# Kernel tuning notes

Hardware: AMD Instinct MI355X
Metric: run time of the kernel (lower is better)

Reference implementation:

```python
import jax, jax.numpy as jnp
import numpy as np

N = 6144
IN_DIM = 256
HID = 64
HEADS = 4
LAT = 32
ALPHA = 0.2  # LeakyReLU negative slope
NEG_INF = -9e15


def setup_inputs() -> dict:
    key = jax.random.key(0)
    ks = jax.random.split(key, 6)
    x = jax.random.normal(ks[0], (N, IN_DIM), jnp.float32)
    # sparse symmetric 0/1 adjacency, avg degree ~ 25
    A = (jax.random.uniform(ks[1], (N, N)) < 0.004).astype(jnp.float32)
    A = jnp.maximum(A, A.T)
    # xavier-uniform-ish params, matching pyGAT GraphAttentionLayer shapes
    s1 = float(np.sqrt(6.0 / (IN_DIM + HID)))
    W_heads = jax.random.uniform(ks[2], (HEADS, IN_DIM, HID), jnp.float32, -s1, s1)
    sa = float(np.sqrt(6.0 / (2 * HID + 1)))
    a_heads = jax.random.uniform(ks[3], (HEADS, 2 * HID), jnp.float32, -sa, sa)
    s2 = float(np.sqrt(6.0 / (HEADS * HID + LAT)))
    W_out = jax.random.uniform(ks[4], (HEADS * HID, LAT), jnp.float32, -s2, s2)
    sb = float(np.sqrt(6.0 / (2 * LAT + 1)))
    a_out = jax.random.uniform(ks[5], (2 * LAT,), jnp.float32, -sb, sb)
    return {"x": x, "A": A, "W_heads": W_heads, "a_heads": a_heads,
            "W_out": W_out, "a_out": a_out}


def _gat_layer(h, adj_mask, W, a, concat):
    # h: [N, F_in], W: [F_in, F], a: [2F]
    Wh = h @ W                              # [N, F]
    f = W.shape[1]
    e_src = Wh @ a[:f]                      # [N]
    e_dst = Wh @ a[f:]                      # [N]
    e = jax.nn.leaky_relu(e_src[:, None] + e_dst[None, :], ALPHA)  # [N, N]
    e = jnp.where(adj_mask, e, NEG_INF)
    att = jax.nn.softmax(e, axis=1)         # masked softmax over neighbors
    out = att @ Wh                          # [N, F]
    return jax.nn.elu(out) if concat else out


def reference(x, A, W_heads, a_heads, W_out, a_out):
    # normalize(A, 'sym', False): D^{-1/2} A D^{-1/2}
    deg = A.sum(axis=1)
    dinv = jnp.where(deg > 0, deg ** -0.5, 0.0)
    An = A * dinv[:, None] * dinv[None, :]
    mask = An > 0
    heads = [_gat_layer(x, mask, W_heads[i], a_heads[i], True) for i in range(HEADS)]
    h = jnp.concatenate(heads, axis=1)      # [N, HEADS*HID]
    z = jax.nn.elu(_gat_layer(h, mask, W_out, a_out, False))  # [N, LAT]
    return jax.nn.sigmoid(z @ z.T)          # [N, N]
```

## Files before the change

kernel.cpp:

```cpp
#include <hip/hip_runtime.h>
#include <hip/hip_bf16.h>

#define NN 6144
#define IN_DIM 256
#define HID 64
#define HEADS 4
#define LAT 32
#define CAP 192
#define ALPHA 0.2f
#define GEMM_BLOCKS 384
#define WSTRIDE 264

typedef __attribute__((ext_vector_type(8))) short bf16x8;
typedef __attribute__((ext_vector_type(4))) float f32x4;

__device__ __forceinline__ float elu_f(float v)   { return v > 0.f ? v : expm1f(v); }
__device__ __forceinline__ float lrelu_f(float v) { return v > 0.f ? v : ALPHA * v; }

__device__ __forceinline__ void split_bf16(float v, unsigned short& hi, unsigned short& lo) {
    unsigned u = __builtin_bit_cast(unsigned, v);
    hi = (unsigned short)(u >> 16);
    float vh = __builtin_bit_cast(float, u & 0xFFFF0000u);
    float rl = v - vh;
    lo = (unsigned short)(__builtin_bit_cast(unsigned, rl) >> 16);
}
__device__ __forceinline__ unsigned short f2bf(float f) {
    unsigned u = __builtin_bit_cast(unsigned, f);
    return (unsigned short)((u + 0x7FFFu + ((u >> 16) & 1u)) >> 16);
}
__device__ __forceinline__ float bf2f(unsigned short b) {
    return __builtin_bit_cast(float, (unsigned)b << 16);
}

__global__ __launch_bounds__(256) void k_pre(const float* __restrict__ A,
                                             const float* __restrict__ x,
                                             const float* __restrict__ Wheads,
                                             const float* __restrict__ aheads,
                                             int* __restrict__ nbr, int* __restrict__ cnt,
                                             unsigned short* __restrict__ Whb,
                                             float* __restrict__ es4, float* __restrict__ ed4) {
    __shared__ __align__(16) float smem[2048];
    int bid = blockIdx.x;
    int t = threadIdx.x;
    if (bid < GEMM_BLOCKS) {
        int head = bid & 3, m0 = (bid >> 2) * 64;
        float (*As)[64] = (float(*)[64])smem;
        float (*Bs)[64] = (float(*)[64])(smem + 1024);
        const float* Wc = Wheads + (size_t)head * IN_DIM * HID;
        int ty = t >> 4, tx = t & 15;
        float acc[4][4] = {};
        for (int k0 = 0; k0 < IN_DIM; k0 += 16) {
            {
                int row = t >> 2, k4 = (t & 3) * 4;
                float4 v = *(const float4*)(x + (size_t)(m0 + row) * IN_DIM + k0 + k4);
                As[k4 + 0][row] = v.x; As[k4 + 1][row] = v.y;
                As[k4 + 2][row] = v.z; As[k4 + 3][row] = v.w;
                int kk = t >> 4, n4 = (t & 15) * 4;
                *(float4*)&Bs[kk][n4] = *(const float4*)(Wc + (size_t)(k0 + kk) * HID + n4);
            }
            __syncthreads();
            #pragma unroll
            for (int k = 0; k < 16; ++k) {
                float4 av = *(float4*)&As[k][ty * 4];
                float4 bv = *(float4*)&Bs[k][tx * 4];
                float ar[4] = {av.x, av.y, av.z, av.w};
                float br[4] = {bv.x, bv.y, bv.z, bv.w};
                #pragma unroll
                for (int i = 0; i < 4; ++i)
                    #pragma unroll
                    for (int j = 0; j < 4; ++j)
                        acc[i][j] = fmaf(ar[i], br[j], acc[i][j]);
            }
            __syncthreads();
        }
        #pragma unroll
        for (int i = 0; i < 4; ++i) {
            ushort4 o;
            o.x = f2bf(acc[i][0]); o.y = f2bf(acc[i][1]);
            o.z = f2bf(acc[i][2]); o.w = f2bf(acc[i][3]);
            *(ushort4*)(Whb + (size_t)(m0 + ty * 4 + i) * (HEADS * HID) + head * HID + tx * 4) = o;
        }
        float4 a1v = *(const float4*)(aheads + head * 2 * HID + tx * 4);
        float4 a2v = *(const float4*)(aheads + head * 2 * HID + HID + tx * 4);
        #pragma unroll
        for (int i = 0; i < 4; ++i) {
            float p1 = acc[i][0] * a1v.x + acc[i][1] * a1v.y + acc[i][2] * a1v.z + acc[i][3] * a1v.w;
            float p2 = acc[i][0] * a2v.x + acc[i][1] * a2v.y + acc[i][2] * a2v.z + acc[i][3] * a2v.w;
            #pragma unroll
            for (int off = 8; off; off >>= 1) {
                p1 += __shfl_down(p1, off, 16);
                p2 += __shfl_down(p2, off, 16);
            }
            if (tx == 0) {
                es4[(size_t)(m0 + ty * 4 + i) * 4 + head] = p1;
                ed4[(size_t)(m0 + ty * 4 + i) * 4 + head] = p2;
            }
        }
    } else {
        int row = bid - GEMM_BLOCKS;
        int* lcnt = (int*)smem;
        const float4* Arow = (const float4*)(A + (size_t)row * NN);
        if (t == 0) *lcnt = 0;
        __syncthreads();
        int* my = nbr + (size_t)row * CAP;
        #pragma unroll
        for (int it = 0; it < NN / 4 / 256; ++it) {
            int idx4 = it * 256 + t;
            float4 v = Arow[idx4];
            int base = idx4 * 4;
            if (v.x != 0.f) { int p = atomicAdd(lcnt, 1); if (p < CAP) my[p] = base; }
            if (v.y != 0.f) { int p = atomicAdd(lcnt, 1); if (p < CAP) my[p] = base + 1; }
            if (v.z != 0.f) { int p = atomicAdd(lcnt, 1); if (p < CAP) my[p] = base + 2; }
            if (v.w != 0.f) { int p = atomicAdd(lcnt, 1); if (p < CAP) my[p] = base + 3; }
        }
        __syncthreads();
        if (t == 0) cnt[row] = *lcnt < CAP ? *lcnt : CAP;
    }
}

__global__ __launch_bounds__(256, 4) void k_attn1g2(const int* __restrict__ nbr, const int* __restrict__ cnt,
                                                    const float4* __restrict__ es4, const float4* __restrict__ ed4,
                                                    const unsigned short* __restrict__ Whb,
                                                    const float* __restrict__ Wout, const float* __restrict__ aout,
                                                    float* __restrict__ Wh2,
                                                    float* __restrict__ es2, float* __restrict__ ed2) {
    __shared__ int colS[4][CAP];
    __shared__ __align__(16) float attH[4][HEADS][CAP];
    __shared__ __align__(16) unsigned short hbf[4][WSTRIDE];
    __shared__ __align__(16) unsigned short WoutT[LAT][WSTRIDE];
    int w = threadIdx.x >> 6, l = threadIdx.x & 63;
    int i = blockIdx.x * 4 + w;
    int c = cnt[i];
    const int* nb = nbr + (size_t)i * CAP;

    #pragma unroll
    for (int it = 0; it < 8; ++it) {
        int q = it * 256 + threadIdx.x;
        float4 v = *(const float4*)(Wout + q * 4);
        int trow = q >> 3, c0 = (q * 4) & 31;
        WoutT[c0 + 0][trow] = f2bf(v.x);
        WoutT[c0 + 1][trow] = f2bf(v.y);
        WoutT[c0 + 2][trow] = f2bf(v.z);
        WoutT[c0 + 3][trow] = f2bf(v.w);
    }

    float4 esv = es4[i];
    float s0 = 0.f, s1 = 0.f, s2 = 0.f, s3 = 0.f;
    for (int j = l; j < c; j += 64) {
        int cj = nb[j];
        colS[w][j] = cj;
        float4 edv = ed4[cj];
        float4 e;
        e.x = __expf(lrelu_f(esv.x + edv.x));
        e.y = __expf(lrelu_f(esv.y + edv.y));
        e.z = __expf(lrelu_f(esv.z + edv.z));
        e.w = __expf(lrelu_f(esv.w + edv.w));
        attH[w][0][j] = e.x; attH[w][1][j] = e.y;
        attH[w][2][j] = e.z; attH[w][3][j] = e.w;
        s0 += e.x; s1 += e.y; s2 += e.z; s3 += e.w;
    }
    #pragma unroll
    for (int off = 32; off; off >>= 1) {
        s0 += __shfl_down(s0, off); s1 += __shfl_down(s1, off);
        s2 += __shfl_down(s2, off); s3 += __shfl_down(s3, off);
    }
    s0 = __shfl(s0, 0); s1 = __shfl(s1, 0); s2 = __shfl(s2, 0); s3 = __shfl(s3, 0);

    int hd = l >> 4;
    float sh = hd < 2 ? (hd == 0 ? s0 : s1) : (hd == 2 ? s2 : s3);
    float invh = 1.0f / sh;
    float4 hv;
    if (c == 0) {
        float a0 = 0.f, a1 = 0.f, a2 = 0.f, a3 = 0.f;
        for (int r = 0; r < NN; ++r) {
            ushort4 v = *(const ushort4*)(Whb + (size_t)r * (HEADS * HID) + 4 * l);
            a0 += bf2f(v.x); a1 += bf2f(v.y); a2 += bf2f(v.z); a3 += bf2f(v.w);
        }
        hv.x = elu_f(a0 / NN); hv.y = elu_f(a1 / NN);
        hv.z = elu_f(a2 / NN); hv.w = elu_f(a3 / NN);
    } else {
        const unsigned short* Wb = Whb + 4 * l;
        float ax[8], ay[8], az[8], aw[8];
        #pragma unroll
        for (int k = 0; k < 8; ++k) { ax[k] = 0.f; ay[k] = 0.f; az[k] = 0.f; aw[k] = 0.f; }
        int j = 0;
        for (; j + 8 <= c; j += 8) {
            float4 f0 = *(float4*)&attH[w][hd][j];
            float4 f1 = *(float4*)&attH[w][hd][j + 4];
            int4 c0v = *(int4*)&colS[w][j];
            int4 c1v = *(int4*)&colS[w][j + 4];
            float ff[8] = {f0.x, f0.y, f0.z, f0.w, f1.x, f1.y, f1.z, f1.w};
            int   cj[8] = {c0v.x, c0v.y, c0v.z, c0v.w, c1v.x, c1v.y, c1v.z, c1v.w};
            ushort4 vv[8];
            #pragma unroll
            for (int k = 0; k < 8; ++k) vv[k] = *(const ushort4*)(Wb + (size_t)cj[k] * (HEADS * HID));
            #pragma unroll
            for (int k = 0; k < 8; ++k) {
                ax[k] = fmaf(ff[k], bf2f(vv[k].x), ax[k]);
                ay[k] = fmaf(ff[k], bf2f(vv[k].y), ay[k]);
                az[k] = fmaf(ff[k], bf2f(vv[k].z), az[k]);
                aw[k] = fmaf(ff[k], bf2f(vv[k].w), aw[k]);
            }
        }
        for (; j < c; ++j) {
            int cj = colS[w][j];
            float f = attH[w][hd][j];
            ushort4 v = *(const ushort4*)(Wb + (size_t)cj * (HEADS * HID));
            ax[0] = fmaf(f, bf2f(v.x), ax[0]); ay[0] = fmaf(f, bf2f(v.y), ay[0]);
            az[0] = fmaf(f, bf2f(v.z), az[0]); aw[0] = fmaf(f, bf2f(v.w), aw[0]);
        }
        float rx = ((ax[0] + ax[1]) + (ax[2] + ax[3])) + ((ax[4] + ax[5]) + (ax[6] + ax[7]));
        float ry = ((ay[0] + ay[1]) + (ay[2] + ay[3])) + ((ay[4] + ay[5]) + (ay[6] + ay[7]));
        float rz = ((az[0] + az[1]) + (az[2] + az[3])) + ((az[4] + az[5]) + (az[6] + az[7]));
        float rw = ((aw[0] + aw[1]) + (aw[2] + aw[3])) + ((aw[4] + aw[5]) + (aw[6] + aw[7]));
        hv.x = elu_f(rx * invh); hv.y = elu_f(ry * invh);
        hv.z = elu_f(rz * invh); hv.w = elu_f(rw * invh);
    }
    {
        ushort4 o;
        o.x = f2bf(hv.x); o.y = f2bf(hv.y); o.z = f2bf(hv.z); o.w = f2bf(hv.w);
        *(ushort4*)&hbf[w][4 * l] = o;
    }
    __syncthreads();

    {
        int r = l & 15, kg = l >> 4;
        f32x4 accA = {0.f, 0.f, 0.f, 0.f};
        f32x4 accB = {0.f, 0.f, 0.f, 0.f};
        #pragma unroll
        for (int k0 = 0; k0 < 8; ++k0) {
            bf16x8 af = {0, 0, 0, 0, 0, 0, 0, 0};
            if (r < 4) af = *(const bf16x8*)&hbf[r][k0 * 32 + kg * 8];
            bf16x8 b0 = *(const bf16x8*)&WoutT[r][k0 * 32 + kg * 8];
            bf16x8 b1 = *(const bf16x8*)&WoutT[16 + r][k0 * 32 + kg * 8];
            accA = __builtin_amdgcn_mfma_f32_16x16x32_bf16(af, b0, accA, 0, 0, 0);
            accB = __builtin_amdgcn_mfma_f32_16x16x32_bf16(af, b1, accB, 0, 0, 0);
        }
        float v0 = (w == 0) ? accA[0] : (w == 1) ? accA[1] : (w == 2) ? accA[2] : accA[3];
        float v1 = (w == 0) ? accB[0] : (w == 1) ? accB[1] : (w == 2) ? accB[2] : accB[3];
        if (l < 16) {
            Wh2[(size_t)i * LAT + l]      = v0;
            Wh2[(size_t)i * LAT + 16 + l] = v1;
            float p1 = v0 * aout[l] + v1 * aout[16 + l];
            float p2 = v0 * aout[32 + l] + v1 * aout[48 + l];
            #pragma unroll
            for (int off = 8; off; off >>= 1) {
                p1 += __shfl_down(p1, off, 16);
                p2 += __shfl_down(p2, off, 16);
            }
            if (l == 0) { es2[i] = p1; ed2[i] = p2; }
        }
    }
}

__global__ __launch_bounds__(256, 8) void k_attn2(const int* __restrict__ nbr, const int* __restrict__ cnt,
                                                  const float* __restrict__ es2, const float* __restrict__ ed2,
                                                  const float* __restrict__ Wh2,
                                                  unsigned short* __restrict__ zh, unsigned short* __restrict__ zl) {
    __shared__ float att[4][CAP];
    __shared__ int col[4][CAP];
    int w = threadIdx.x >> 6, l = threadIdx.x & 63;
    int i = blockIdx.x * 4 + w;
    int c = cnt[i];
    if (c == 0) {
        if (l < LAT) {
            float s = 0.f;
            for (int r = 0; r < NN; ++r) s += Wh2[(size_t)r * LAT + l];
            unsigned short hi, lo;
            split_bf16(elu_f(s * (1.0f / NN)), hi, lo);
            zh[(size_t)i * LAT + l] = hi;
            zl[(size_t)i * LAT + l] = lo;
        }
        return;
    }
    float esi = es2[i];
    const int* nb = nbr + (size_t)i * CAP;
    float s = 0.f;
    for (int j = l; j < c; j += 64) {
        int cj = nb[j];
        col[w][j] = cj;
        float p = __expf(lrelu_f(esi + ed2[cj]));
        att[w][j] = p;
        s += p;
    }
    #pragma unroll
    for (int off = 32; off; off >>= 1) s += __shfl_down(s, off);
    s = __shfl(s, 0);
    if (l < LAT) {
        float inv = 1.0f / s;
        float a0 = 0.f, a1 = 0.f, a2 = 0.f, a3 = 0.f;
        int j = 0;
        for (; j + 4 <= c; j += 4) {
            a0 = fmaf(att[w][j + 0], Wh2[(size_t)col[w][j + 0] * LAT + l], a0);
            a1 = fmaf(att[w][j + 1], Wh2[(size_t)col[w][j + 1] * LAT + l], a1);
            a2 = fmaf(att[w][j + 2], Wh2[(size_t)col[w][j + 2] * LAT + l], a2);
            a3 = fmaf(att[w][j + 3], Wh2[(size_t)col[w][j + 3] * LAT + l], a3);
        }
        for (; j < c; ++j)
            a0 = fmaf(att[w][j], Wh2[(size_t)col[w][j] * LAT + l], a0);
        unsigned short hi, lo;
        split_bf16(elu_f(((a0 + a1) + (a2 + a3)) * inv), hi, lo);
        zh[(size_t)i * LAT + l] = hi;
        zl[(size_t)i * LAT + l] = lo;
    }
}

__global__ __launch_bounds__(256, 8) void k_zzt(const unsigned short* __restrict__ zh,
                                                const unsigned short* __restrict__ zl,
                                                float* __restrict__ out) {
    int t = threadIdx.x, w = t >> 6, l = t & 63;
    int m0 = blockIdx.y * 64 + w * 16;
    int n0 = blockIdx.x * 64;
    int r = l & 15, kg = (l >> 4) * 8;
    bf16x8 ah = *(const bf16x8*)(zh + (size_t)(m0 + r) * LAT + kg);
    bf16x8 al = *(const bf16x8*)(zl + (size_t)(m0 + r) * LAT + kg);
    int mbase = m0 + (l >> 4) * 4;
    #pragma unroll
    for (int jp = 0; jp < 2; ++jp) {
        int nbA = n0 + (jp * 2 + 0) * 16;
        int nbB = n0 + (jp * 2 + 1) * 16;
        bf16x8 bhA = *(const bf16x8*)(zh + (size_t)(nbA + r) * LAT + kg);
        bf16x8 blA = *(const bf16x8*)(zl + (size_t)(nbA + r) * LAT + kg);
        bf16x8 bhB = *(const bf16x8*)(zh + (size_t)(nbB + r) * LAT + kg);
        bf16x8 blB = *(const bf16x8*)(zl + (size_t)(nbB + r) * LAT + kg);
        f32x4 accA = {0.f, 0.f, 0.f, 0.f};
        accA = __builtin_amdgcn_mfma_f32_16x16x32_bf16(ah, bhA, accA, 0, 0, 0);
        accA = __builtin_amdgcn_mfma_f32_16x16x32_bf16(ah, blA, accA, 0, 0, 0);
        accA = __builtin_amdgcn_mfma_f32_16x16x32_bf16(al, bhA, accA, 0, 0, 0);
        f32x4 accB = {0.f, 0.f, 0.f, 0.f};
        accB = __builtin_amdgcn_mfma_f32_16x16x32_bf16(ah, bhB, accB, 0, 0, 0);
        accB = __builtin_amdgcn_mfma_f32_16x16x32_bf16(ah, blB, accB, 0, 0, 0);
        accB = __builtin_amdgcn_mfma_f32_16x16x32_bf16(al, bhB, accB, 0, 0, 0);
        float4 oA, oB;
        oA.x = 1.0f / (1.0f + __expf(-accA[0]));
        oA.y = 1.0f / (1.0f + __expf(-accA[1]));
        oA.z = 1.0f / (1.0f + __expf(-accA[2]));
        oA.w = 1.0f / (1.0f + __expf(-accA[3]));
        oB.x = 1.0f / (1.0f + __expf(-accB[0]));
        oB.y = 1.0f / (1.0f + __expf(-accB[1]));
        oB.z = 1.0f / (1.0f + __expf(-accB[2]));
        oB.w = 1.0f / (1.0f + __expf(-accB[3]));
        *(float4*)(out + (size_t)(nbA + (l & 15)) * NN + mbase) = oA;
        *(float4*)(out + (size_t)(nbB + (l & 15)) * NN + mbase) = oB;
    }
}

extern "C" void kernel_launch(void* const* d_in, const int* in_sizes, int n_in,
                              void* d_out, int out_size, void* d_ws, size_t ws_size,
                              hipStream_t stream) {
    const float* x      = (const float*)d_in[0];
    const float* A      = (const float*)d_in[1];
    const float* Wheads = (const float*)d_in[2];
    const float* aheads = (const float*)d_in[3];
    const float* Wout   = (const float*)d_in[4];
    const float* aout   = (const float*)d_in[5];
    float* out = (float*)d_out;

    char* ws = (char*)d_ws;
    size_t o = 0;
    auto alloc = [&](size_t bytes) { void* p = ws + o; o += (bytes + 255) & ~(size_t)255; return p; };
    int*   nbr   = (int*)  alloc((size_t)NN * CAP * 4);
    int*   cnt   = (int*)  alloc((size_t)NN * 4);
    unsigned short* Whb = (unsigned short*)alloc((size_t)NN * HEADS * HID * 2);
    float* es4   = (float*)alloc((size_t)NN * 4 * 4);
    float* ed4   = (float*)alloc((size_t)NN * 4 * 4);
    float* Wh2   = (float*)alloc((size_t)NN * LAT * 4);
    float* es2   = (float*)alloc((size_t)NN * 4);
    float* ed2   = (float*)alloc((size_t)NN * 4);
    unsigned short* zh = (unsigned short*)alloc((size_t)NN * LAT * 2);
    unsigned short* zl = (unsigned short*)alloc((size_t)NN * LAT * 2);

    k_pre     <<<GEMM_BLOCKS + NN, 256, 0, stream>>>(A, x, Wheads, aheads, nbr, cnt, Whb, es4, ed4);
    k_attn1g2 <<<NN / 4, 256, 0, stream>>>(nbr, cnt, (const float4*)es4, (const float4*)ed4,
                                           Whb, Wout, aout, Wh2, es2, ed2);
    k_attn2   <<<NN / 4, 256, 0, stream>>>(nbr, cnt, es2, ed2, Wh2, zh, zl);
    k_zzt     <<<dim3(NN / 64, NN / 64), 256, 0, stream>>>(zh, zl, out);
}
```

Measured before the change: 108.1 us.

## Precompute bf16 Wout transpose in k_pre and shrink attention blocks to two waves

The bf16 transpose of Wout moves out of every k_attn1g2 block into one extra k_pre block that writes it to global memory once. k_attn1g2 then uses 128-thread blocks (two rows), keeps attention weights as bf16 in shared memory, drops the block barrier, reads Wout tiles straight from global/L2, and uses a 4-way instead of 8-way gather unroll. The aim is to cut redundant per-block transpose work and shared-memory footprint so occupancy rises. The trade-offs are extra rounding of attention weights to bf16, less memory-level parallelism per wave in the gather, and MFMA B operands fetched from global instead of LDS.

```diff
diff --git a/kernel.cpp b/kernel.cpp
--- a/kernel.cpp
+++ b/kernel.cpp
@@ -9,7 +9,6 @@
 #define CAP 192
 #define ALPHA 0.2f
 #define GEMM_BLOCKS 384
-#define WSTRIDE 264
 
 typedef __attribute__((ext_vector_type(8))) short bf16x8;
 typedef __attribute__((ext_vector_type(4))) float f32x4;
@@ -36,9 +35,11 @@
                                              const float* __restrict__ x,
                                              const float* __restrict__ Wheads,
                                              const float* __restrict__ aheads,
+                                             const float* __restrict__ Wout,
                                              int* __restrict__ nbr, int* __restrict__ cnt,
                                              unsigned short* __restrict__ Whb,
-                                             float* __restrict__ es4, float* __restrict__ ed4) {
+                                             float* __restrict__ es4, float* __restrict__ ed4,
+                                             unsigned short* __restrict__ WoutT) {
     __shared__ __align__(16) float smem[2048];
     int bid = blockIdx.x;
     int t = threadIdx.x;
@@ -96,7 +97,7 @@
                 ed4[(size_t)(m0 + ty * 4 + i) * 4 + head] = p2;
             }
         }
-    } else {
+    } else if (bid < GEMM_BLOCKS + NN) {
         int row = bid - GEMM_BLOCKS;
         int* lcnt = (int*)smem;
         const float4* Arow = (const float4*)(A + (size_t)row * NN);
@@ -115,34 +116,32 @@
         }
         __syncthreads();
         if (t == 0) cnt[row] = *lcnt < CAP ? *lcnt : CAP;
-    }
-}
-
-__global__ __launch_bounds__(256, 4) void k_attn1g2(const int* __restrict__ nbr, const int* __restrict__ cnt,
+    } else {
+        #pragma unroll
+        for (int cq = 0; cq < 8; ++cq) {
+            float4 v = *(const float4*)(Wout + t * LAT + cq * 4);
+            WoutT[(cq * 4 + 0) * IN_DIM + t] = f2bf(v.x);
+            WoutT[(cq * 4 + 1) * IN_DIM + t] = f2bf(v.y);
+            WoutT[(cq * 4 + 2) * IN_DIM + t] = f2bf(v.z);
+            WoutT[(cq * 4 + 3) * IN_DIM + t] = f2bf(v.w);
+        }
+    }
+}
+
+__global__ __launch_bounds__(128, 8) void k_attn1g2(const int* __restrict__ nbr, const int* __restrict__ cnt,
                                                     const float4* __restrict__ es4, const float4* __restrict__ ed4,
                                                     const unsigned short* __restrict__ Whb,
-                                                    const float* __restrict__ Wout, const float* __restrict__ aout,
+                                                    const unsigned short* __restrict__ WoutT,
+                                                    const float* __restrict__ aout,
                                                     float* __restrict__ Wh2,
                                                     float* __restrict__ es2, float* __restrict__ ed2) {
-    __shared__ int colS[4][CAP];
-    __shared__ __align__(16) float attH[4][HEADS][CAP];
-    __shared__ __align__(16) unsigned short hbf[4][WSTRIDE];
-    __shared__ __align__(16) unsigned short WoutT[LAT][WSTRIDE];
+    __shared__ int colS[2][CAP];
+    __shared__ __align__(16) unsigned short attB[2][HEADS][CAP];
+    __shared__ __align__(16) unsigned short hr[2][HEADS * HID];
     int w = threadIdx.x >> 6, l = threadIdx.x & 63;
-    int i = blockIdx.x * 4 + w;
+    int i = blockIdx.x * 2 + w;
     int c = cnt[i];
     const int* nb = nbr + (size_t)i * CAP;
-
-    #pragma unroll
-    for (int it = 0; it < 8; ++it) {
-        int q = it * 256 + threadIdx.x;
-        float4 v = *(const float4*)(Wout + q * 4);
-        int trow = q >> 3, c0 = (q * 4) & 31;
-        WoutT[c0 + 0][trow] = f2bf(v.x);
-        WoutT[c0 + 1][trow] = f2bf(v.y);
-        WoutT[c0 + 2][trow] = f2bf(v.z);
-        WoutT[c0 + 3][trow] = f2bf(v.w);
-    }
 
     float4 esv = es4[i];
     float s0 = 0.f, s1 = 0.f, s2 = 0.f, s3 = 0.f;
@@ -150,14 +149,13 @@
         int cj = nb[j];
         colS[w][j] = cj;
         float4 edv = ed4[cj];
-        float4 e;
-        e.x = __expf(lrelu_f(esv.x + edv.x));
-        e.y = __expf(lrelu_f(esv.y + edv.y));
-        e.z = __expf(lrelu_f(esv.z + edv.z));
-        e.w = __expf(lrelu_f(esv.w + edv.w));
-        attH[w][0][j] = e.x; attH[w][1][j] = e.y;
-        attH[w][2][j] = e.z; attH[w][3][j] = e.w;
-        s0 += e.x; s1 += e.y; s2 += e.z; s3 += e.w;
+        float ex = __expf(lrelu_f(esv.x + edv.x));
+        float ey = __expf(lrelu_f(esv.y + edv.y));
+        float ez = __expf(lrelu_f(esv.z + edv.z));
+        float ew = __expf(lrelu_f(esv.w + edv.w));
+        attB[w][0][j] = f2bf(ex); attB[w][1][j] = f2bf(ey);
+        attB[w][2][j] = f2bf(ez); attB[w][3][j] = f2bf(ew);
+        s0 += ex; s1 += ey; s2 += ez; s3 += ew;
     }
     #pragma unroll
     for (int off = 32; off; off >>= 1) {
@@ -180,22 +178,20 @@
         hv.z = elu_f(a2 / NN); hv.w = elu_f(a3 / NN);
     } else {
         const unsigned short* Wb = Whb + 4 * l;
-        float ax[8], ay[8], az[8], aw[8];
-        #pragma unroll
-        for (int k = 0; k < 8; ++k) { ax[k] = 0.f; ay[k] = 0.f; az[k] = 0.f; aw[k] = 0.f; }
+        float ax[4], ay[4], az[4], aw[4];
+        #pragma unroll
+        for (int k = 0; k < 4; ++k) { ax[k] = 0.f; ay[k] = 0.f; az[k] = 0.f; aw[k] = 0.f; }
         int j = 0;
-        for (; j + 8 <= c; j += 8) {
-            float4 f0 = *(float4*)&attH[w][hd][j];
-            float4 f1 = *(float4*)&attH[w][hd][j + 4];
-            int4 c0v = *(int4*)&colS[w][j];
-            int4 c1v = *(int4*)&colS[w][j + 4];
-            float ff[8] = {f0.x, f0.y, f0.z, f0.w, f1.x, f1.y, f1.z, f1.w};
-            int   cj[8] = {c0v.x, c0v.y, c0v.z, c0v.w, c1v.x, c1v.y, c1v.z, c1v.w};
-            ushort4 vv[8];
-            #pragma unroll
-            for (int k = 0; k < 8; ++k) vv[k] = *(const ushort4*)(Wb + (size_t)cj[k] * (HEADS * HID));
-            #pragma unroll
-            for (int k = 0; k < 8; ++k) {
+        for (; j + 4 <= c; j += 4) {
+            ushort4 fB = *(ushort4*)&attB[w][hd][j];
+            int4 cv = *(int4*)&colS[w][j];
+            float ff[4] = {bf2f(fB.x), bf2f(fB.y), bf2f(fB.z), bf2f(fB.w)};
+            int   cj[4] = {cv.x, cv.y, cv.z, cv.w};
+            ushort4 vv[4];
+            #pragma unroll
+            for (int k = 0; k < 4; ++k) vv[k] = *(const ushort4*)(Wb + (size_t)cj[k] * (HEADS * HID));
+            #pragma unroll
+            for (int k = 0; k < 4; ++k) {
                 ax[k] = fmaf(ff[k], bf2f(vv[k].x), ax[k]);
                 ay[k] = fmaf(ff[k], bf2f(vv[k].y), ay[k]);
                 az[k] = fmaf(ff[k], bf2f(vv[k].z), az[k]);
@@ -204,24 +200,21 @@
         }
         for (; j < c; ++j) {
             int cj = colS[w][j];
-            float f = attH[w][hd][j];
+            float f = bf2f(attB[w][hd][j]);
             ushort4 v = *(const ushort4*)(Wb + (size_t)cj * (HEADS * HID));
             ax[0] = fmaf(f, bf2f(v.x), ax[0]); ay[0] = fmaf(f, bf2f(v.y), ay[0]);
             az[0] = fmaf(f, bf2f(v.z), az[0]); aw[0] = fmaf(f, bf2f(v.w), aw[0]);
         }
-        float rx = ((ax[0] + ax[1]) + (ax[2] + ax[3])) + ((ax[4] + ax[5]) + (ax[6] + ax[7]));
-        float ry = ((ay[0] + ay[1]) + (ay[2] + ay[3])) + ((ay[4] + ay[5]) + (ay[6] + ay[7]));
-        float rz = ((az[0] + az[1]) + (az[2] + az[3])) + ((az[4] + az[5]) + (az[6] + az[7]));
-        float rw = ((aw[0] + aw[1]) + (aw[2] + aw[3])) + ((aw[4] + aw[5]) + (aw[6] + aw[7]));
-        hv.x = elu_f(rx * invh); hv.y = elu_f(ry * invh);
-        hv.z = elu_f(rz * invh); hv.w = elu_f(rw * invh);
+        hv.x = elu_f(((ax[0] + ax[1]) + (ax[2] + ax[3])) * invh);
+        hv.y = elu_f(((ay[0] + ay[1]) + (ay[2] + ay[3])) * invh);
+        hv.z = elu_f(((az[0] + az[1]) + (az[2] + az[3])) * invh);
+        hv.w = elu_f(((aw[0] + aw[1]) + (aw[2] + aw[3])) * invh);
     }
     {
         ushort4 o;
         o.x = f2bf(hv.x); o.y = f2bf(hv.y); o.z = f2bf(hv.z); o.w = f2bf(hv.w);
-        *(ushort4*)&hbf[w][4 * l] = o;
-    }
-    __syncthreads();
+        *(ushort4*)&hr[w][4 * l] = o;
+    }
 
     {
         int r = l & 15, kg = l >> 4;
@@ -230,15 +223,14 @@
         #pragma unroll
         for (int k0 = 0; k0 < 8; ++k0) {
             bf16x8 af = {0, 0, 0, 0, 0, 0, 0, 0};
-            if (r < 4) af = *(const bf16x8*)&hbf[r][k0 * 32 + kg * 8];
-            bf16x8 b0 = *(const bf16x8*)&WoutT[r][k0 * 32 + kg * 8];
-            bf16x8 b1 = *(const bf16x8*)&WoutT[16 + r][k0 * 32 + kg * 8];
+            if (r == 0) af = *(const bf16x8*)&hr[w][k0 * 32 + kg * 8];
+            bf16x8 b0 = *(const bf16x8*)(WoutT + (size_t)r * IN_DIM + k0 * 32 + kg * 8);
+            bf16x8 b1 = *(const bf16x8*)(WoutT + (size_t)(16 + r) * IN_DIM + k0 * 32 + kg * 8);
             accA = __builtin_amdgcn_mfma_f32_16x16x32_bf16(af, b0, accA, 0, 0, 0);
             accB = __builtin_amdgcn_mfma_f32_16x16x32_bf16(af, b1, accB, 0, 0, 0);
         }
-        float v0 = (w == 0) ? accA[0] : (w == 1) ? accA[1] : (w == 2) ? accA[2] : accA[3];
-        float v1 = (w == 0) ? accB[0] : (w == 1) ? accB[1] : (w == 2) ? accB[2] : accB[3];
         if (l < 16) {
+            float v0 = accA[0], v1 = accB[0];
             Wh2[(size_t)i * LAT + l]      = v0;
             Wh2[(size_t)i * LAT + 16 + l] = v1;
             float p1 = v0 * aout[l] + v1 * aout[16 + l];
@@ -369,10 +361,12 @@
     float* ed2   = (float*)alloc((size_t)NN * 4);
     unsigned short* zh = (unsigned short*)alloc((size_t)NN * LAT * 2);
     unsigned short* zl = (unsigned short*)alloc((size_t)NN * LAT * 2);
-
-    k_pre     <<<GEMM_BLOCKS + NN, 256, 0, stream>>>(A, x, Wheads, aheads, nbr, cnt, Whb, es4, ed4);
-    k_attn1g2 <<<NN / 4, 256, 0, stream>>>(nbr, cnt, (const float4*)es4, (const float4*)ed4,
-                                           Whb, Wout, aout, Wh2, es2, ed2);
+    unsigned short* WoutT = (unsigned short*)alloc((size_t)LAT * IN_DIM * 2);
+
+    k_pre     <<<GEMM_BLOCKS + NN + 1, 256, 0, stream>>>(A, x, Wheads, aheads, Wout,
+                                                         nbr, cnt, Whb, es4, ed4, WoutT);
+    k_attn1g2 <<<NN / 2, 128, 0, stream>>>(nbr, cnt, (const float4*)es4, (const float4*)ed4,
+                                           Whb, WoutT, aout, Wh2, es2, ed2);
     k_attn2   <<<NN / 4, 256, 0, stream>>>(nbr, cnt, es2, ed2, Wh2, zh, zl);
     k_zzt     <<<dim3(NN / 64, NN / 64), 256, 0, stream>>>(zh, zl, out);
 }
```

New measurement: 111.1 us. +2.8%, slower.
